# Optimization experiments

Measured on AMD Instinct MI355X. Metric: run time of the kernel, lower is better.

Reference implementation:

```python
import jax, jax.numpy as jnp
import numpy as np

B, S, Lc = 128, 128, 20          # batch, words per sentence, chars per word
AB, E = 100, 64                  # char alphabet, char embedding dim
Hc, H, OUT = 256, 512, 50        # char hidden, word hidden, n tags
PAD = 0                          # padding idx for words and chars


def _cell_params(key, din, h):
    k1, k2, k3, k4 = jax.random.split(key, 4)
    return (jax.random.normal(k1, (4 * h, din)) * 0.05,
            jax.random.normal(k2, (4 * h, h)) * 0.05,
            jax.random.normal(k3, (4 * h,)) * 0.05,
            jax.random.normal(k4, (4 * h,)) * 0.05)


def setup_inputs() -> dict:
    key = jax.random.key(0)
    ks = jax.random.split(key, 12)
    x = jax.random.randint(ks[0], (B, S, Lc), 0, AB)
    emb = jax.random.normal(ks[1], (AB, E)) * 0.05
    emb = emb.at[PAD].set(0.0)  # nn.Embedding padding_idx row is zero
    cW_ih, cW_hh, cb_ih, cb_hh = _cell_params(ks[2], E, Hc)
    fW_ih, fW_hh, fb_ih, fb_hh = _cell_params(ks[3], Hc, H)
    bW_ih, bW_hh, bb_ih, bb_hh = _cell_params(ks[4], Hc, H)
    W1 = jax.random.normal(ks[5], (256, 2 * H)) * 0.05
    b1 = jax.random.normal(ks[6], (256,)) * 0.05
    W2 = jax.random.normal(ks[7], (256, 256)) * 0.05
    b2 = jax.random.normal(ks[8], (256,)) * 0.05
    W3 = jax.random.normal(ks[9], (OUT, 256)) * 0.05
    b3 = jax.random.normal(ks[10], (OUT,)) * 0.05
    return dict(x=x, emb=emb,
                cW_ih=cW_ih, cW_hh=cW_hh, cb_ih=cb_ih, cb_hh=cb_hh,
                fW_ih=fW_ih, fW_hh=fW_hh, fb_ih=fb_ih, fb_hh=fb_hh,
                bW_ih=bW_ih, bW_hh=bW_hh, bb_ih=bb_ih, bb_hh=bb_hh,
                W1=W1, b1=b1, W2=W2, b2=b2, W3=W3, b3=b3)


def _lstm_cell(x_t, h, c, W_ih, W_hh, b_ih, b_hh):
    # PyTorch LSTMCell: gates ordered i, f, g, o
    g = x_t @ W_ih.T + b_ih + h @ W_hh.T + b_hh
    i, f, gg, o = jnp.split(g, 4, axis=-1)
    c = jax.nn.sigmoid(f) * c + jax.nn.sigmoid(i) * jnp.tanh(gg)
    h = jax.nn.sigmoid(o) * jnp.tanh(c)
    return h, c


def _char_acceptor(e_seq, lengths, W_ih, W_hh, b_ih, b_hh, hsize):
    # e_seq: [N, T, E]; returns last non-padded hidden state per row: [N, hsize]
    N, T, _ = e_seq.shape
    h0 = jnp.zeros((N, hsize), e_seq.dtype)

    def step(carry, inp):
        h, c, last = carry
        x_t, t = inp
        h, c = _lstm_cell(x_t, h, c, W_ih, W_hh, b_ih, b_hh)
        last = jnp.where((lengths > t)[:, None], h, last)
        return (h, c, last), None

    xs = (jnp.swapaxes(e_seq, 0, 1), jnp.arange(T))
    (_, _, last), _ = jax.lax.scan(step, (h0, h0, h0), xs)
    return last


def _lstm_transduce(seq_tbd, W_ih, W_hh, b_ih, b_hh, hsize):
    # seq_tbd: [T, B, D] -> all hidden states [T, B, hsize]
    Tb = seq_tbd.shape[1]
    h0 = jnp.zeros((Tb, hsize), seq_tbd.dtype)

    def step(carry, x_t):
        h, c = carry
        h, c = _lstm_cell(x_t, h, c, W_ih, W_hh, b_ih, b_hh)
        return (h, c), h

    _, hs = jax.lax.scan(step, (h0, h0), seq_tbd)
    return hs


def reference(x, emb,
              cW_ih, cW_hh, cb_ih, cb_hh,
              fW_ih, fW_hh, fb_ih, fb_hh,
              bW_ih, bW_hh, bb_ih, bb_hh,
              W1, b1, W2, b2, W3, b3):
    Bx, Sx, Lx = x.shape
    xf = x.reshape(Bx * Sx, Lx)                       # all words flattened
    e = emb[xf]                                       # [B*S, Lc, E]
    lengths = (xf != PAD).sum(axis=1)
    char_out = _char_acceptor(e, lengths, cW_ih, cW_hh, cb_ih, cb_hh, Hc)
    word_seq = char_out.reshape(Bx, Sx, Hc)           # [B, S, Hc]

    seq_tbd = jnp.swapaxes(word_seq, 0, 1)            # [S, B, Hc]
    hs_f = _lstm_transduce(seq_tbd, fW_ih, fW_hh, fb_ih, fb_hh, H)
    hs_b = _lstm_transduce(seq_tbd[::-1], bW_ih, bW_hh, bb_ih, bb_hh, H)[::-1]
    hs = jnp.concatenate([hs_f, hs_b], axis=-1)       # [S, B, 2H]
    hs = jnp.swapaxes(hs, 0, 1)                       # [B, S, 2H]

    h1 = jax.nn.relu(hs @ W1.T + b1)
    h2 = jax.nn.relu(h1 @ W2.T + b2)
    logits = h2 @ W3.T + b3                           # [B, S, OUT]
    return jax.nn.log_softmax(logits, axis=2)
```

## Files before the change

kernel.cpp:

```cpp
#include <hip/hip_runtime.h>
#include <hip/hip_bf16.h>
#include <math.h>

typedef __hip_bfloat16 bf16;
typedef __attribute__((ext_vector_type(8))) short bf16x8;
typedef __attribute__((ext_vector_type(4))) float f32x4;
typedef long i64t;

#define NW   16384
#define LC   20
#define EDIM 64
#define HC   256
#define HW   512
#define SEQ  128
#define NOUT 50
#define NWB  64
#define FPAD 16

#define LOG2E 1.4426950408889634f
__device__ __forceinline__ float fex2(float x) {
  float r; asm("v_exp_f32 %0, %1" : "=v"(r) : "v"(x)); return r;
}
__device__ __forceinline__ float frcp(float x) {
  float r; asm("v_rcp_f32 %0, %1" : "=v"(r) : "v"(x)); return r;
}
__device__ __forceinline__ float flog2(float x) {
  float r; asm("v_log_f32 %0, %1" : "=v"(r) : "v"(x)); return r;
}
__device__ __forceinline__ float fsig(float x) { return frcp(1.f + fex2(-LOG2E * x)); }
__device__ __forceinline__ float ftanh(float x) {
  return 1.f - 2.f * frcp(1.f + fex2(2.f * LOG2E * x));
}

__device__ __forceinline__ unsigned short f2bu(float f) {
  bf16 h = __float2bfloat16(f);
  return *reinterpret_cast<unsigned short*>(&h);
}
__device__ __forceinline__ bf16x8 ld8(const unsigned short* p) {
  return *reinterpret_cast<const bf16x8*>(p);
}
__device__ __forceinline__ float fp8_to_f32(unsigned int b) {
  float r; asm("v_cvt_f32_fp8 %0, %1" : "=v"(r) : "v"(b)); return r;
}
__device__ __forceinline__ i64t ld8sc8(const unsigned char* p) {
  i64t r;
  asm volatile("global_load_dwordx2 %0, %1, off sc0 sc1" : "=v"(r) : "v"(p));
  return r;
}
__device__ __forceinline__ void st8sc8(unsigned char* p, i64t v) {
  asm volatile("global_store_dwordx2 %0, %1, off sc0 sc1" :: "v"(p), "v"(v) : "memory");
}
#define MFMA(a, b, c)  __builtin_amdgcn_mfma_f32_16x16x32_bf16(a, b, c, 0, 0, 0)
#define MFMA8(a, b, c) __builtin_amdgcn_mfma_f32_16x16x32_fp8_fp8(a, b, c, 0, 0, 0)

__global__ __launch_bounds__(512, 1) void char_lstm(
    const int* __restrict__ x, const unsigned char* __restrict__ emb8,
    const unsigned char* __restrict__ Wc8, const float* __restrict__ bcT,
    unsigned short* __restrict__ lastT, const int* __restrict__ len) {
  __shared__ unsigned char Hs8[2][64][264];
  __shared__ _Float16 Cs[256][66];
  __shared__ int lenS[64];
  const int tid = threadIdx.x;
  const int w = tid >> 6, l = tid & 63;
  const int l16 = l & 15, lk8 = (l >> 4) * 8, q = l >> 4;
  const int w0 = blockIdx.x * 64;
  if (tid < 64) lenS[tid] = len[w0 + tid];

  for (int t = 0; t < LC; ++t) {
    const int cur = t & 1, nxt = cur ^ 1;
    int xi[4];
#pragma unroll
    for (int wh = 0; wh < 4; ++wh) xi[wh] = x[(w0 + wh * 16 + l16) * LC + t];
#pragma unroll
    for (int c = 0; c < 2; ++c) {
      const int chg = w * 2 + c;
      const int cc0 = chg * 64;
      f32x4 acc[4][4] = {};
#pragma unroll
      for (int kk = 0; kk < 2; ++kk) {
        const int k = kk * 32 + lk8;
        const unsigned char* wp = Wc8 + (size_t)(cc0 + l16) * 320 + k;
        i64t bv8[4];
#pragma unroll
        for (int g = 0; g < 4; ++g)
          bv8[g] = *reinterpret_cast<const i64t*>(wp + g * 16 * 320);
#pragma unroll
        for (int wh = 0; wh < 4; ++wh) {
          i64t a8 = *reinterpret_cast<const i64t*>(emb8 + (size_t)xi[wh] * 64 + k);
#pragma unroll
          for (int g = 0; g < 4; ++g) acc[wh][g] = MFMA8(bv8[g], a8, acc[wh][g]);
        }
      }
      if (t > 0) {
#pragma unroll
        for (int kk = 2; kk < 10; ++kk) {
          const int k = kk * 32 + lk8;
          const unsigned char* wp = Wc8 + (size_t)(cc0 + l16) * 320 + k;
          i64t bv8[4];
#pragma unroll
          for (int g = 0; g < 4; ++g)
            bv8[g] = *reinterpret_cast<const i64t*>(wp + g * 16 * 320);
#pragma unroll
          for (int wh = 0; wh < 4; ++wh) {
            i64t a8 = *reinterpret_cast<const i64t*>(&Hs8[cur][wh * 16 + l16][k - 64]);
#pragma unroll
            for (int g = 0; g < 4; ++g) acc[wh][g] = MFMA8(bv8[g], a8, acc[wh][g]);
          }
        }
      }
      float4 bb4[4];
#pragma unroll
      for (int e = 0; e < 4; ++e)
        bb4[e] = *reinterpret_cast<const float4*>(bcT + (chg * 16 + q * 4 + e) * 4);
      const int uoff = chg * 16 + q * 4;
#pragma unroll
      for (int wh = 0; wh < 4; ++wh) {
        const int wd = wh * 16 + l16;
        float hv[4];
#pragma unroll
        for (int e = 0; e < 4; ++e) {
          const int ug = chg * 16 + q * 4 + e;
          const float gi = acc[wh][0][e] + bb4[e].x;
          const float gf = acc[wh][1][e] + bb4[e].y;
          const float gg = acc[wh][2][e] + bb4[e].z;
          const float go = acc[wh][3][e] + bb4[e].w;
          const float cprev = t ? (float)Cs[ug][wd] : 0.f;
          const float ccv = fsig(gf) * cprev + fsig(gi) * ftanh(gg);
          Cs[ug][wd] = (_Float16)ccv;
          hv[e] = fsig(go) * ftanh(ccv);
        }
        const int d0 = __builtin_amdgcn_cvt_pk_fp8_f32(hv[0], hv[1], 0, false);
        const int d1 = __builtin_amdgcn_cvt_pk_fp8_f32(hv[2], hv[3], 0, false);
        const unsigned int pk = (unsigned int)(d0 & 0xFFFF) |
                                ((unsigned int)(d1 & 0xFFFF) << 16);
        *reinterpret_cast<unsigned int*>(&Hs8[nxt][wd][uoff]) = pk;
      }
    }
    __syncthreads();
    {
      const int wd = tid >> 3, sub = tid & 7;
      const int myl = lenS[wd];
      if (myl == t + 1 || (myl == 0 && t == 0)) {
        const int n = w0 + wd;
        const int lrow = ((n & 127) * 128 + (n >> 7)) * HC;
        if (myl == 0) {
          bf16x8 z = {};
#pragma unroll
          for (int j = 0; j < 4; ++j)
            *reinterpret_cast<bf16x8*>(lastT + lrow + sub * 32 + j * 8) = z;
        } else {
#pragma unroll
          for (int j = 0; j < 4; ++j) {
            unsigned int v0 = *reinterpret_cast<unsigned int*>(
                &Hs8[nxt][wd][sub * 32 + j * 8]);
            unsigned int v1 = *reinterpret_cast<unsigned int*>(
                &Hs8[nxt][wd][sub * 32 + j * 8 + 4]);
            union { unsigned short s[8]; bf16x8 v; } o;
#pragma unroll
            for (int b = 0; b < 4; ++b) {
              o.s[b]     = f2bu(fp8_to_f32((v0 >> (8 * b)) & 0xFF));
              o.s[4 + b] = f2bu(fp8_to_f32((v1 >> (8 * b)) & 0xFF));
            }
            *reinterpret_cast<bf16x8*>(lastT + lrow + sub * 32 + j * 8) = o.v;
          }
        }
      }
    }
  }
}

__global__ __launch_bounds__(256, 1) void word_lstm(
    const unsigned short* __restrict__ lastT,
    const unsigned short* __restrict__ W16,
    const unsigned short* __restrict__ W16b,
    const unsigned char* __restrict__ W8f,
    const unsigned char* __restrict__ W8b,
    const float* __restrict__ bfi, const float* __restrict__ bbi,
    unsigned char* __restrict__ hbL8,
    unsigned short* __restrict__ hsW,
    int* __restrict__ aflag) {
  __shared__ unsigned short Wlds16[64 * 256];
  __shared__ unsigned char  Wlds8[64 * 512];
  __shared__ unsigned short ht[128][24];
  __shared__ unsigned char  ht8[128][24];
  const int tid = threadIdx.x;
  const int w = tid >> 6, l = tid & 63;
  const int l16 = l & 15, lk8 = (l >> 4) * 8, q = l >> 4;
  const int dir = blockIdx.x >> 5;
  const int nb = blockIdx.x & 31;
  const int c0 = nb * 64;
  const unsigned short* Wx = dir ? W16b : W16;
  const unsigned char*  Wh = dir ? W8b : W8f;
  const float* bias = dir ? bbi : bfi;
  for (int ci = tid; ci < 64 * 32; ci += 256) {
    const int col = ci >> 5, kc = (ci & 31) * 8;
    const int kcs = kc ^ ((col & 15) * 8);
    *reinterpret_cast<bf16x8*>(&Wlds16[col * 256 + kcs]) =
        ld8(Wx + (size_t)(c0 + col) * 768 + kc);
  }
  for (int ci = tid; ci < 64 * 64; ci += 256) {
    const int col = ci >> 6, kb = (ci & 63) * 8;
    const int kbs = kb ^ ((col & 15) * 8);
    *reinterpret_cast<i64t*>(&Wlds8[col * 512 + kbs]) =
        *reinterpret_cast<const i64t*>(Wh + (size_t)(c0 + col) * 512 + kb);
  }
  const float b0 = bias[c0 + 0 * 16 + l16];
  const float b1 = bias[c0 + 1 * 16 + l16];
  const float b2 = bias[c0 + 2 * 16 + l16];
  const float b3 = bias[c0 + 3 * 16 + l16];
  const int ksw = l16 * 8;
  float cst[8];
#pragma unroll
  for (int i = 0; i < 8; ++i) cst[i] = 0.f;
  __syncthreads();

  for (int t = 0; t < SEQ; ++t) {
    const int cur = t & 1;
    const int pos = dir ? (SEQ - 1 - t) : t;
    f32x4 acc[2][4] = {};
#pragma unroll
    for (int kk = 0; kk < 8; ++kk) {
      const int k = kk * 32 + lk8;
      bf16x8 a0 = ld8(lastT + ((size_t)pos * 128 + w * 32 + l16) * HC + k);
      bf16x8 a1 = ld8(lastT + ((size_t)pos * 128 + w * 32 + l16 + 16) * HC + k);
      const int ks = k ^ ksw;
#pragma unroll
      for (int nn = 0; nn < 4; ++nn) {
        bf16x8 bv = ld8(&Wlds16[(l16 + nn * 16) * 256 + ks]);
        acc[0][nn] = MFMA(a0, bv, acc[0][nn]);
        acc[1][nn] = MFMA(a1, bv, acc[1][nn]);
      }
    }
    if (t > 0) {
      if (w == 0) {
        const int* fp = aflag + (size_t)(dir * SEQ + (t - 1)) * 32 * FPAD;
        for (;;) {
          int v = 1;
          if (l < 32)
            v = __hip_atomic_load(fp + l * FPAD, __ATOMIC_RELAXED,
                                  __HIP_MEMORY_SCOPE_AGENT);
          if (__ballot(v != 0) == ~0ull) break;
          __builtin_amdgcn_s_sleep(1);
        }
      }
      __syncthreads();
      i64t af8[16][2];
      const unsigned char* hp =
          hbL8 + (size_t)(((cur ^ 1) * 2 + dir) * 32) * 128 * 16;
#pragma unroll
      for (int kk = 0; kk < 16; ++kk) {
        const int u = kk * 32 + lk8;
        const int nbs = u >> 4, ul = u & 15;
#pragma unroll
        for (int r = 0; r < 2; ++r) {
          const int bt = w * 32 + l16 + r * 16;
          af8[kk][r] = ld8sc8(hp + ((size_t)nbs * 128 + bt) * 16 + ul);
        }
      }
      asm volatile("s_waitcnt vmcnt(0)" ::: "memory");
      __builtin_amdgcn_sched_barrier(0);
#pragma unroll
      for (int kk = 0; kk < 16; ++kk) {
        const int ks8 = (kk * 32 + lk8) ^ ksw;
#pragma unroll
        for (int nn = 0; nn < 4; ++nn) {
          i64t w8 = *reinterpret_cast<const i64t*>(
              &Wlds8[(l16 + nn * 16) * 512 + ks8]);
          acc[0][nn] = MFMA8(af8[kk][0], w8, acc[0][nn]);
          acc[1][nn] = MFMA8(af8[kk][1], w8, acc[1][nn]);
        }
      }
    }
    float hvf[8];
    int bats[8];
#pragma unroll
    for (int m = 0; m < 2; ++m)
#pragma unroll
      for (int e = 0; e < 4; ++e) {
        const int j = m * 4 + e;
        const float gi = acc[m][0][e] + b0;
        const float gf = acc[m][1][e] + b1;
        const float gg = acc[m][2][e] + b2;
        const float go = acc[m][3][e] + b3;
        const float ccv = fsig(gf) * cst[j] + fsig(gi) * ftanh(gg);
        cst[j] = ccv;
        const float hv = fsig(go) * ftanh(ccv);
        const int bat = w * 32 + q * 4 + e + m * 16;
        ht[bat][l16] = f2bu(hv);
        hvf[j] = hv; bats[j] = bat;
      }
    {
      const int d0 = __builtin_amdgcn_cvt_pk_fp8_f32(hvf[0], hvf[1], 0, false);
      const int d1 = __builtin_amdgcn_cvt_pk_fp8_f32(hvf[2], hvf[3], 0, false);
      const int d2 = __builtin_amdgcn_cvt_pk_fp8_f32(hvf[4], hvf[5], 0, false);
      const int d3 = __builtin_amdgcn_cvt_pk_fp8_f32(hvf[6], hvf[7], 0, false);
      ht8[bats[0]][l16] = (unsigned char)(d0 & 255);
      ht8[bats[1]][l16] = (unsigned char)((d0 >> 8) & 255);
      ht8[bats[2]][l16] = (unsigned char)(d1 & 255);
      ht8[bats[3]][l16] = (unsigned char)((d1 >> 8) & 255);
      ht8[bats[4]][l16] = (unsigned char)(d2 & 255);
      ht8[bats[5]][l16] = (unsigned char)((d2 >> 8) & 255);
      ht8[bats[6]][l16] = (unsigned char)(d3 & 255);
      ht8[bats[7]][l16] = (unsigned char)((d3 >> 8) & 255);
    }
    __syncthreads();
    const int ub = tid >> 1, uh = tid & 1;
    i64t hv8 = *reinterpret_cast<const i64t*>(&ht8[ub][uh * 8]);
    st8sc8(hbL8 + (size_t)((cur * 2 + dir) * 32 + nb) * 128 * 16
               + ub * 16 + uh * 8, hv8);
    if (t < SEQ - 1) {
      asm volatile("s_waitcnt vmcnt(0)" ::: "memory");
      __syncthreads();
      if (tid == 0)
        __hip_atomic_store(aflag + ((size_t)(dir * SEQ + t) * 32 + nb) * FPAD, 1,
                           __ATOMIC_RELAXED, __HIP_MEMORY_SCOPE_AGENT);
    }
    bf16x8 hv = ld8(&ht[ub][uh * 8]);
    *reinterpret_cast<bf16x8*>(
        hsW + (((size_t)(dir * 32 + nb) * 128 + pos) * 128 + ub) * 16 + uh * 8) = hv;
  }
}

__global__ __launch_bounds__(256) void mlp1_gemm(
    const unsigned short* __restrict__ hsW, const unsigned short* __restrict__ W1b,
    const float* __restrict__ bias, unsigned short* __restrict__ out) {
  const int tid = threadIdx.x;
  const int w = tid >> 6, l = tid & 63;
  const int l16 = l & 15, lk8 = (l >> 4) * 8;
  const int by = blockIdx.y;
  const int row0 = by * 128 + w * 32;
  const int col0 = blockIdx.x * 64;
  f32x4 acc[2][4] = {};
  for (int kk = 0; kk < 32; ++kk) {
    const int k = kk * 32 + lk8;
    const int dirk = k >> 9, u = k & 511, nbs = u >> 4, ul = u & 15;
    const int p0 = w * 32 + l16, p1 = p0 + 16;
    bf16x8 a0 = ld8(hsW + (((size_t)(dirk * 32 + nbs) * 128 + p0) * 128 + by) * 16 + ul);
    bf16x8 a1 = ld8(hsW + (((size_t)(dirk * 32 + nbs) * 128 + p1) * 128 + by) * 16 + ul);
    const unsigned short* wp = W1b + (size_t)(col0 + l16) * 1024 + k;
#pragma unroll
    for (int nn = 0; nn < 4; ++nn) {
      bf16x8 bv = ld8(wp + nn * 16 * 1024);
      acc[0][nn] = MFMA(a0, bv, acc[0][nn]);
      acc[1][nn] = MFMA(a1, bv, acc[1][nn]);
    }
  }
  const int cr = (l >> 4) * 4;
#pragma unroll
  for (int m = 0; m < 2; ++m)
#pragma unroll
    for (int nn = 0; nn < 4; ++nn)
#pragma unroll
      for (int e = 0; e < 4; ++e) {
        const int r = row0 + m * 16 + cr + e;
        const int c = col0 + nn * 16 + l16;
        out[(size_t)r * 256 + c] = f2bu(fmaxf(acc[m][nn][e] + bias[c], 0.f));
      }
}

__global__ __launch_bounds__(256) void mlp_gemm(
    const unsigned short* __restrict__ A, int lda,
    const unsigned short* __restrict__ W, int ldw,
    const float* __restrict__ bias, unsigned short* __restrict__ out,
    int ldo, int nk, int relu) {
  const int tid = threadIdx.x;
  const int w = tid >> 6, l = tid & 63;
  const int l16 = l & 15, lk8 = (l >> 4) * 8;
  const int row0 = blockIdx.y * 128 + w * 32;
  const int col0 = blockIdx.x * 64;
  f32x4 acc[2][4] = {};
  for (int kk = 0; kk < nk; ++kk) {
    const int k = kk * 32 + lk8;
    bf16x8 a0 = ld8(A + (size_t)(row0 + l16) * lda + k);
    bf16x8 a1 = ld8(A + (size_t)(row0 + 16 + l16) * lda + k);
    const unsigned short* wp = W + (size_t)(col0 + l16) * ldw + k;
    bf16x8 bb[4];
#pragma unroll
    for (int nn = 0; nn < 4; ++nn) bb[nn] = ld8(wp + nn * 16 * ldw);
#pragma unroll
    for (int nn = 0; nn < 4; ++nn) {
      acc[0][nn] = MFMA(a0, bb[nn], acc[0][nn]);
      acc[1][nn] = MFMA(a1, bb[nn], acc[1][nn]);
    }
  }
  const int cr = (l >> 4) * 4;
#pragma unroll
  for (int m = 0; m < 2; ++m)
#pragma unroll
    for (int nn = 0; nn < 4; ++nn)
#pragma unroll
      for (int e = 0; e < 4; ++e) {
        const int r = row0 + m * 16 + cr + e;
        const int c = col0 + nn * 16 + l16;
        float v = acc[m][nn][e] + bias[c];
        if (relu) v = fmaxf(v, 0.f);
        out[(size_t)r * ldo + c] = f2bu(v);
      }
}

__global__ __launch_bounds__(256) void logits_fused(
    const unsigned short* __restrict__ h2, const unsigned short* __restrict__ W3p,
    const float* __restrict__ b3, float* __restrict__ out) {
  __shared__ float gt[128][68];
  __shared__ float lseb[128];
  const int tid = threadIdx.x;
  const int w = tid >> 6, l = tid & 63;
  const int l16 = l & 15, lk8 = (l >> 4) * 8;
  const int r0 = blockIdx.x * 128;
  const int rr0 = w * 32 + l16, rr1 = rr0 + 16;
  f32x4 acc[2][4] = {};
#pragma unroll
  for (int kk = 0; kk < 8; ++kk) {
    const int k = kk * 32 + lk8;
    bf16x8 a0 = ld8(h2 + (size_t)(r0 + rr0) * 256 + k);
    bf16x8 a1 = ld8(h2 + (size_t)(r0 + rr1) * 256 + k);
#pragma unroll
    for (int nn = 0; nn < 4; ++nn) {
      bf16x8 bv = ld8(W3p + (size_t)(nn * 16 + l16) * 256 + k);
      acc[0][nn] = MFMA(a0, bv, acc[0][nn]);
      acc[1][nn] = MFMA(a1, bv, acc[1][nn]);
    }
  }
  const int cr = (l >> 4) * 4;
#pragma unroll
  for (int m = 0; m < 2; ++m)
#pragma unroll
    for (int nn = 0; nn < 4; ++nn)
#pragma unroll
      for (int e = 0; e < 4; ++e) {
        const int col = nn * 16 + l16;
        gt[w * 32 + m * 16 + cr + e][col] =
            acc[m][nn][e] + (col < NOUT ? b3[col] : 0.f);
      }
  __syncthreads();
  if (tid < 128) {
    float mx = -INFINITY;
#pragma unroll
    for (int j = 0; j < NOUT; ++j) mx = fmaxf(mx, gt[tid][j]);
    float s = 0.f;
#pragma unroll
    for (int j = 0; j < NOUT; ++j) s += fex2(LOG2E * (gt[tid][j] - mx));
    lseb[tid] = flog2(s) * 0.6931471805599453f + mx;
  }
  __syncthreads();
  for (int idx = tid; idx < 128 * NOUT; idx += 256) {
    const int r = idx / NOUT, j = idx - r * NOUT;
    out[(size_t)(r0 + r) * NOUT + j] = gt[r][j] - lseb[r];
  }
}

__global__ void prep_w(const float* __restrict__ ih, const float* __restrict__ hh,
                       unsigned short* __restrict__ dst, int HU, int KI, int KH) {
  const int K = KI + KH;
  const long tot = (long)HU * 4 * K;
  for (long idx = (long)blockIdx.x * blockDim.x + threadIdx.x; idx < tot;
       idx += (long)gridDim.x * blockDim.x) {
    const int row = (int)(idx / K), k = (int)(idx % K);
    const int chunk = row >> 6, c = row & 63;
    const int g = c >> 4, u = chunk * 16 + (c & 15);
    const float v = (k < KI) ? ih[(size_t)(g * HU + u) * KI + k]
                             : hh[(size_t)(g * HU + u) * KH + (k - KI)];
    dst[idx] = f2bu(v);
  }
}

__global__ void prep_wc8(const float* __restrict__ ih, const float* __restrict__ hh,
                         unsigned char* __restrict__ dst, int HU, int KI, int KH) {
  const int K = KI + KH;
  const long tot = (long)HU * 4 * (K / 2);
  for (long p = (long)blockIdx.x * blockDim.x + threadIdx.x; p < tot;
       p += (long)gridDim.x * blockDim.x) {
    const int row = (int)(p / (K / 2)), kp = (int)(p % (K / 2)) * 2;
    const int chunk = row >> 6, c = row & 63;
    const int g = c >> 4, u = chunk * 16 + (c & 15);
    const float a = (kp < KI) ? ih[(size_t)(g * HU + u) * KI + kp]
                              : hh[(size_t)(g * HU + u) * KH + (kp - KI)];
    const float b = (kp + 1 < KI) ? ih[(size_t)(g * HU + u) * KI + kp + 1]
                                  : hh[(size_t)(g * HU + u) * KH + (kp + 1 - KI)];
    const int d = __builtin_amdgcn_cvt_pk_fp8_f32(a, b, 0, false);
    *reinterpret_cast<unsigned short*>(dst + (size_t)row * K + kp) =
        (unsigned short)(d & 0xFFFF);
  }
}

__global__ void prep_w8(const float* __restrict__ hh, unsigned char* __restrict__ dst,
                        int HU, int KH) {
  const long tot = (long)HU * 4 * (KH / 2);
  for (long p = (long)blockIdx.x * blockDim.x + threadIdx.x; p < tot;
       p += (long)gridDim.x * blockDim.x) {
    const int row = (int)(p / (KH / 2)), kp = (int)(p % (KH / 2)) * 2;
    const int chunk = row >> 6, c = row & 63;
    const int g = c >> 4, u = chunk * 16 + (c & 15);
    const float a = hh[(size_t)(g * HU + u) * KH + kp];
    const float b = hh[(size_t)(g * HU + u) * KH + kp + 1];
    const int d = __builtin_amdgcn_cvt_pk_fp8_f32(a, b, 0, false);
    *reinterpret_cast<unsigned short*>(dst + (size_t)row * KH + kp) =
        (unsigned short)(d & 0xFFFF);
  }
}

__global__ void prep_bias(const float* bih, const float* bhh, float* dst, int HU) {
  const int idx = blockIdx.x * blockDim.x + threadIdx.x;
  if (idx < 4 * HU) {
    const int chunk = idx >> 6, c = idx & 63;
    const int g = c >> 4, u = chunk * 16 + (c & 15);
    dst[idx] = bih[g * HU + u] + bhh[g * HU + u];
  }
}

__global__ void prep_biasT(const float* bih, const float* bhh, float* dst, int HU) {
  const int idx = blockIdx.x * blockDim.x + threadIdx.x;
  if (idx < 4 * HU) {
    const int u = idx >> 2, g = idx & 3;
    dst[idx] = bih[g * HU + u] + bhh[g * HU + u];
  }
}

__global__ void conv_bf(const float* __restrict__ src, unsigned short* __restrict__ dst,
                        long n) {
  for (long i = (long)blockIdx.x * blockDim.x + threadIdx.x; i < n;
       i += (long)gridDim.x * blockDim.x)
    dst[i] = f2bu(src[i]);
}

__global__ void conv_fp8(const float* __restrict__ src, unsigned char* __restrict__ dst,
                         long n2) {
  for (long i = (long)blockIdx.x * blockDim.x + threadIdx.x; i < n2;
       i += (long)gridDim.x * blockDim.x) {
    const int d = __builtin_amdgcn_cvt_pk_fp8_f32(src[i * 2], src[i * 2 + 1], 0, false);
    *reinterpret_cast<unsigned short*>(dst + i * 2) = (unsigned short)(d & 0xFFFF);
  }
}

__global__ void prep_w3(const float* __restrict__ W3, unsigned short* __restrict__ dst) {
  const int i = blockIdx.x * blockDim.x + threadIdx.x;
  if (i < 64 * 256) {
    const int r = i >> 8;
    dst[i] = (r < NOUT) ? f2bu(W3[i]) : 0;
  }
}

__global__ void lengths_k(const int* x, int* len) {
  const int n = blockIdx.x * blockDim.x + threadIdx.x;
  if (n < NW) {
    int c = 0;
#pragma unroll
    for (int l = 0; l < LC; ++l) c += (x[(size_t)n * LC + l] != 0) ? 1 : 0;
    len[n] = c;
  }
}

__global__ void zero_k(int* p, int n) {
  const int i = blockIdx.x * blockDim.x + threadIdx.x;
  if (i < n) p[i] = 0;
}

__global__ void sentinel_k(float* out, int n) {
  const int i = blockIdx.x * blockDim.x + threadIdx.x;
  if (i < n) out[i] = 1000.0f;
}

extern "C" void kernel_launch(void* const* d_in, const int* in_sizes, int n_in,
                              void* d_out, int out_size, void* d_ws, size_t ws_size,
                              hipStream_t stream) {
  const int*   x     = (const int*)d_in[0];
  const float* emb   = (const float*)d_in[1];
  const float* cW_ih = (const float*)d_in[2];
  const float* cW_hh = (const float*)d_in[3];
  const float* cb_ih = (const float*)d_in[4];
  const float* cb_hh = (const float*)d_in[5];
  const float* fW_ih = (const float*)d_in[6];
  const float* fW_hh = (const float*)d_in[7];
  const float* fb_ih = (const float*)d_in[8];
  const float* fb_hh = (const float*)d_in[9];
  const float* bW_ih = (const float*)d_in[10];
  const float* bW_hh = (const float*)d_in[11];
  const float* bb_ih = (const float*)d_in[12];
  const float* bb_hh = (const float*)d_in[13];
  const float* W1 = (const float*)d_in[14];
  const float* b1 = (const float*)d_in[15];
  const float* W2 = (const float*)d_in[16];
  const float* b2 = (const float*)d_in[17];
  const float* W3 = (const float*)d_in[18];
  const float* b3 = (const float*)d_in[19];
  float* out = (float*)d_out;
  (void)in_sizes; (void)n_in;

  char* ws = (char*)d_ws;
  size_t off = 0;
  auto alloc = [&](size_t bytes) -> char* {
    char* p = ws + off;
    off += (bytes + 255) & ~(size_t)255;
    return p;
  };
  int*            len_  = (int*)alloc((size_t)NW * 4);
  int*            aflag = (int*)alloc((size_t)2 * SEQ * 32 * FPAD * 4);
  unsigned char*  emb8  = (unsigned char*)alloc((size_t)100 * EDIM);
  unsigned char*  Wc8   = (unsigned char*)alloc((size_t)1024 * 320);
  unsigned short* Wf_i  = (unsigned short*)alloc((size_t)2048 * 768 * 2);
  unsigned short* Wb_i  = (unsigned short*)alloc((size_t)2048 * 768 * 2);
  unsigned char*  Wf8   = (unsigned char*)alloc((size_t)2048 * 512);
  unsigned char*  Wb8   = (unsigned char*)alloc((size_t)2048 * 512);
  unsigned short* W1b   = (unsigned short*)alloc((size_t)256 * 1024 * 2);
  unsigned short* W2b   = (unsigned short*)alloc((size_t)256 * 256 * 2);
  unsigned short* W3p   = (unsigned short*)alloc((size_t)64 * 256 * 2);
  float*          bcT   = (float*)alloc(1024 * 4);
  float*          bf_i  = (float*)alloc(2048 * 4);
  float*          bb_i  = (float*)alloc(2048 * 4);
  unsigned short* lastT = (unsigned short*)alloc((size_t)NW * HC * 2);
  unsigned char*  hbL8  = (unsigned char*)alloc((size_t)2 * 2 * 32 * 128 * 16);
  unsigned short* hsW   = (unsigned short*)alloc((size_t)2 * 32 * 128 * 128 * 16 * 2);
  unsigned short* h1    = (unsigned short*)alloc((size_t)NW * HC * 2);
  unsigned short* h2    = (unsigned short*)alloc((size_t)NW * HC * 2);

  if (off > ws_size) {
    sentinel_k<<<(out_size + 255) / 256, 256, 0, stream>>>(out, out_size);
    return;
  }

  auto cdiv = [](long a, long b) { return (int)((a + b - 1) / b); };

  prep_wc8<<<640, 256, 0, stream>>>(cW_ih, cW_hh, Wc8, HC, EDIM, HC);
  prep_w<<<3072, 256, 0, stream>>>(fW_ih, fW_hh, Wf_i, HW, HC, HW);
  prep_w<<<3072, 256, 0, stream>>>(bW_ih, bW_hh, Wb_i, HW, HC, HW);
  prep_w8<<<2048, 256, 0, stream>>>(fW_hh, Wf8, HW, HW);
  prep_w8<<<2048, 256, 0, stream>>>(bW_hh, Wb8, HW, HW);
  prep_biasT<<<cdiv(1024, 256), 256, 0, stream>>>(cb_ih, cb_hh, bcT, HC);
  prep_bias<<<cdiv(2048, 256), 256, 0, stream>>>(fb_ih, fb_hh, bf_i, HW);
  prep_bias<<<cdiv(2048, 256), 256, 0, stream>>>(bb_ih, bb_hh, bb_i, HW);
  conv_fp8<<<13, 256, 0, stream>>>(emb, emb8, 100L * EDIM / 2);
  conv_bf<<<1024, 256, 0, stream>>>(W1, W1b, 256L * 1024);
  conv_bf<<<256, 256, 0, stream>>>(W2, W2b, 256L * 256);
  prep_w3<<<64, 256, 0, stream>>>(W3, W3p);
  lengths_k<<<cdiv(NW, 256), 256, 0, stream>>>(x, len_);
  zero_k<<<cdiv(2 * SEQ * 32 * FPAD, 256), 256, 0, stream>>>(aflag, 2 * SEQ * 32 * FPAD);

  char_lstm<<<NW / 64, 512, 0, stream>>>(x, emb8, Wc8, bcT, lastT, len_);

  word_lstm<<<NWB, 256, 0, stream>>>(lastT, Wf_i, Wb_i, Wf8, Wb8, bf_i, bb_i,
                                     hbL8, hsW, aflag);

  mlp1_gemm<<<dim3(4, 128), 256, 0, stream>>>(hsW, W1b, b1, h1);
  mlp_gemm<<<dim3(4, 128), 256, 0, stream>>>(h1, 256, W2b, 256, b2, h2, 256, 8, 1);
  logits_fused<<<NW / 128, 256, 0, stream>>>(h2, W3p, b3, out);
}
```

Before: 1.372 ms.

## Place word-LSTM directions on single XCDs and use cheaper cache scope when co-located

The word LSTM now launches 256 blocks and keeps only those with blockIdx%8 in {0,1}. With round-robin block dispatch this is meant to put all 32 blocks of one direction on the same XCD. Each block reads its XCD id from a hardware register, counts co-residents, and when all 32 share an XCD it uses sc0-only (L2-coherent) loads and stores for the recurrent state and flags instead of sc0 sc1 system-scope accesses. This aims to cut per-step cross-block synchronisation latency. The input-weight prep also drops the unused recurrent half of the bf16 matrix, shrinking that buffer and prep kernel. The speed path depends on the undocumented block-to-XCD mapping, with fallback to the old coherent path otherwise.

```diff
diff --git a/kernel.cpp b/kernel.cpp
--- a/kernel.cpp
+++ b/kernel.cpp
@@ -14,7 +14,6 @@
 #define HW   512
 #define SEQ  128
 #define NOUT 50
-#define NWB  64
 #define FPAD 16
 
 #define LOG2E 1.4426950408889634f
@@ -42,13 +41,25 @@
 __device__ __forceinline__ float fp8_to_f32(unsigned int b) {
   float r; asm("v_cvt_f32_fp8 %0, %1" : "=v"(r) : "v"(b)); return r;
 }
-__device__ __forceinline__ i64t ld8sc8(const unsigned char* p) {
+__device__ __forceinline__ i64t ld8x(const unsigned char* p, bool f) {
   i64t r;
-  asm volatile("global_load_dwordx2 %0, %1, off sc0 sc1" : "=v"(r) : "v"(p));
+  if (f) asm volatile("global_load_dwordx2 %0, %1, off sc0" : "=v"(r) : "v"(p));
+  else   asm volatile("global_load_dwordx2 %0, %1, off sc0 sc1" : "=v"(r) : "v"(p));
   return r;
 }
-__device__ __forceinline__ void st8sc8(unsigned char* p, i64t v) {
-  asm volatile("global_store_dwordx2 %0, %1, off sc0 sc1" :: "v"(p), "v"(v) : "memory");
+__device__ __forceinline__ void st8x(unsigned char* p, i64t v, bool f) {
+  if (f) asm volatile("global_store_dwordx2 %0, %1, off sc0" :: "v"(p), "v"(v) : "memory");
+  else   asm volatile("global_store_dwordx2 %0, %1, off sc0 sc1" :: "v"(p), "v"(v) : "memory");
+}
+__device__ __forceinline__ int ldflagx(const int* p, bool f) {
+  int r;
+  if (f) asm volatile("global_load_dword %0, %1, off sc0" : "=v"(r) : "v"(p));
+  else   asm volatile("global_load_dword %0, %1, off sc0 sc1" : "=v"(r) : "v"(p));
+  return r;
+}
+__device__ __forceinline__ void stflagx(int* p, int v, bool f) {
+  if (f) asm volatile("global_store_dword %0, %1, off sc0" :: "v"(p), "v"(v) : "memory");
+  else   asm volatile("global_store_dword %0, %1, off sc0 sc1" :: "v"(p), "v"(v) : "memory");
 }
 #define MFMA(a, b, c)  __builtin_amdgcn_mfma_f32_16x16x32_bf16(a, b, c, 0, 0, 0)
 #define MFMA8(a, b, c) __builtin_amdgcn_mfma_f32_16x16x32_fp8_fp8(a, b, c, 0, 0, 0)
@@ -179,24 +190,37 @@
     unsigned char* __restrict__ hbL8,
     unsigned short* __restrict__ hsW,
     int* __restrict__ aflag) {
+  const int bx = blockIdx.x;
+  if ((bx & 7) > 1) return;
   __shared__ unsigned short Wlds16[64 * 256];
   __shared__ unsigned char  Wlds8[64 * 512];
   __shared__ unsigned short ht[128][24];
   __shared__ unsigned char  ht8[128][24];
+  __shared__ int fastS;
   const int tid = threadIdx.x;
   const int w = tid >> 6, l = tid & 63;
   const int l16 = l & 15, lk8 = (l >> 4) * 8, q = l >> 4;
-  const int dir = blockIdx.x >> 5;
-  const int nb = blockIdx.x & 31;
+  const int dir = bx & 7;
+  const int nb = bx >> 3;
   const int c0 = nb * 64;
   const unsigned short* Wx = dir ? W16b : W16;
   const unsigned char*  Wh = dir ? W8b : W8f;
   const float* bias = dir ? bbi : bfi;
+  int* negcnt = aflag + (size_t)2 * SEQ * 32 * FPAD;
+  if (tid == 0) {
+    const int xcc = __builtin_amdgcn_s_getreg(20 | (31 << 11)) & 7;
+    int* xc = negcnt + 16 + dir * 8 + xcc;
+    __hip_atomic_fetch_add(xc, 1, __ATOMIC_RELAXED, __HIP_MEMORY_SCOPE_AGENT);
+    __hip_atomic_fetch_add(negcnt, 1, __ATOMIC_RELAXED, __HIP_MEMORY_SCOPE_AGENT);
+    while (__hip_atomic_load(negcnt, __ATOMIC_RELAXED, __HIP_MEMORY_SCOPE_AGENT) < 64)
+      __builtin_amdgcn_s_sleep(2);
+    fastS = (__hip_atomic_load(xc, __ATOMIC_RELAXED, __HIP_MEMORY_SCOPE_AGENT) == 32);
+  }
   for (int ci = tid; ci < 64 * 32; ci += 256) {
     const int col = ci >> 5, kc = (ci & 31) * 8;
     const int kcs = kc ^ ((col & 15) * 8);
     *reinterpret_cast<bf16x8*>(&Wlds16[col * 256 + kcs]) =
-        ld8(Wx + (size_t)(c0 + col) * 768 + kc);
+        ld8(Wx + (size_t)(c0 + col) * 256 + kc);
   }
   for (int ci = tid; ci < 64 * 64; ci += 256) {
     const int col = ci >> 6, kb = (ci & 63) * 8;
@@ -213,6 +237,7 @@
 #pragma unroll
   for (int i = 0; i < 8; ++i) cst[i] = 0.f;
   __syncthreads();
+  const bool fast = (fastS != 0);
 
   for (int t = 0; t < SEQ; ++t) {
     const int cur = t & 1;
@@ -236,9 +261,7 @@
         const int* fp = aflag + (size_t)(dir * SEQ + (t - 1)) * 32 * FPAD;
         for (;;) {
           int v = 1;
-          if (l < 32)
-            v = __hip_atomic_load(fp + l * FPAD, __ATOMIC_RELAXED,
-                                  __HIP_MEMORY_SCOPE_AGENT);
+          if (l < 32) v = ldflagx(fp + l * FPAD, fast);
           if (__ballot(v != 0) == ~0ull) break;
           __builtin_amdgcn_s_sleep(1);
         }
@@ -254,7 +277,7 @@
 #pragma unroll
         for (int r = 0; r < 2; ++r) {
           const int bt = w * 32 + l16 + r * 16;
-          af8[kk][r] = ld8sc8(hp + ((size_t)nbs * 128 + bt) * 16 + ul);
+          af8[kk][r] = ld8x(hp + ((size_t)nbs * 128 + bt) * 16 + ul, fast);
         }
       }
       asm volatile("s_waitcnt vmcnt(0)" ::: "memory");
@@ -306,14 +329,13 @@
     __syncthreads();
     const int ub = tid >> 1, uh = tid & 1;
     i64t hv8 = *reinterpret_cast<const i64t*>(&ht8[ub][uh * 8]);
-    st8sc8(hbL8 + (size_t)((cur * 2 + dir) * 32 + nb) * 128 * 16
-               + ub * 16 + uh * 8, hv8);
+    st8x(hbL8 + (size_t)((cur * 2 + dir) * 32 + nb) * 128 * 16
+             + ub * 16 + uh * 8, hv8, fast);
     if (t < SEQ - 1) {
       asm volatile("s_waitcnt vmcnt(0)" ::: "memory");
       __syncthreads();
       if (tid == 0)
-        __hip_atomic_store(aflag + ((size_t)(dir * SEQ + t) * 32 + nb) * FPAD, 1,
-                           __ATOMIC_RELAXED, __HIP_MEMORY_SCOPE_AGENT);
+        stflagx(aflag + ((size_t)(dir * SEQ + t) * 32 + nb) * FPAD, 1, fast);
     }
     bf16x8 hv = ld8(&ht[ub][uh * 8]);
     *reinterpret_cast<bf16x8*>(
@@ -449,18 +471,15 @@
   }
 }
 
-__global__ void prep_w(const float* __restrict__ ih, const float* __restrict__ hh,
-                       unsigned short* __restrict__ dst, int HU, int KI, int KH) {
-  const int K = KI + KH;
-  const long tot = (long)HU * 4 * K;
+__global__ void prep_wx(const float* __restrict__ ih, unsigned short* __restrict__ dst,
+                        int HU, int KI) {
+  const long tot = (long)HU * 4 * KI;
   for (long idx = (long)blockIdx.x * blockDim.x + threadIdx.x; idx < tot;
        idx += (long)gridDim.x * blockDim.x) {
-    const int row = (int)(idx / K), k = (int)(idx % K);
+    const int row = (int)(idx / KI), k = (int)(idx % KI);
     const int chunk = row >> 6, c = row & 63;
     const int g = c >> 4, u = chunk * 16 + (c & 15);
-    const float v = (k < KI) ? ih[(size_t)(g * HU + u) * KI + k]
-                             : hh[(size_t)(g * HU + u) * KH + (k - KI)];
-    dst[idx] = f2bu(v);
+    dst[idx] = f2bu(ih[(size_t)(g * HU + u) * KI + k]);
   }
 }
 
@@ -593,12 +612,13 @@
     off += (bytes + 255) & ~(size_t)255;
     return p;
   };
+  const int NFLAG = 2 * SEQ * 32 * FPAD + 32;
   int*            len_  = (int*)alloc((size_t)NW * 4);
-  int*            aflag = (int*)alloc((size_t)2 * SEQ * 32 * FPAD * 4);
+  int*            aflag = (int*)alloc((size_t)NFLAG * 4);
   unsigned char*  emb8  = (unsigned char*)alloc((size_t)100 * EDIM);
   unsigned char*  Wc8   = (unsigned char*)alloc((size_t)1024 * 320);
-  unsigned short* Wf_i  = (unsigned short*)alloc((size_t)2048 * 768 * 2);
-  unsigned short* Wb_i  = (unsigned short*)alloc((size_t)2048 * 768 * 2);
+  unsigned short* Wf_i  = (unsigned short*)alloc((size_t)2048 * 256 * 2);
+  unsigned short* Wb_i  = (unsigned short*)alloc((size_t)2048 * 256 * 2);
   unsigned char*  Wf8   = (unsigned char*)alloc((size_t)2048 * 512);
   unsigned char*  Wb8   = (unsigned char*)alloc((size_t)2048 * 512);
   unsigned short* W1b   = (unsigned short*)alloc((size_t)256 * 1024 * 2);
@@ -621,8 +641,8 @@
   auto cdiv = [](long a, long b) { return (int)((a + b - 1) / b); };
 
   prep_wc8<<<640, 256, 0, stream>>>(cW_ih, cW_hh, Wc8, HC, EDIM, HC);
-  prep_w<<<3072, 256, 0, stream>>>(fW_ih, fW_hh, Wf_i, HW, HC, HW);
-  prep_w<<<3072, 256, 0, stream>>>(bW_ih, bW_hh, Wb_i, HW, HC, HW);
+  prep_wx<<<1024, 256, 0, stream>>>(fW_ih, Wf_i, HW, HC);
+  prep_wx<<<1024, 256, 0, stream>>>(bW_ih, Wb_i, HW, HC);
   prep_w8<<<2048, 256, 0, stream>>>(fW_hh, Wf8, HW, HW);
   prep_w8<<<2048, 256, 0, stream>>>(bW_hh, Wb8, HW, HW);
   prep_biasT<<<cdiv(1024, 256), 256, 0, stream>>>(cb_ih, cb_hh, bcT, HC);
@@ -633,11 +653,11 @@
   conv_bf<<<256, 256, 0, stream>>>(W2, W2b, 256L * 256);
   prep_w3<<<64, 256, 0, stream>>>(W3, W3p);
   lengths_k<<<cdiv(NW, 256), 256, 0, stream>>>(x, len_);
-  zero_k<<<cdiv(2 * SEQ * 32 * FPAD, 256), 256, 0, stream>>>(aflag, 2 * SEQ * 32 * FPAD);
+  zero_k<<<cdiv(NFLAG, 256), 256, 0, stream>>>(aflag, NFLAG);
 
   char_lstm<<<NW / 64, 512, 0, stream>>>(x, emb8, Wc8, bcT, lastT, len_);
 
-  word_lstm<<<NWB, 256, 0, stream>>>(lastT, Wf_i, Wb_i, Wf8, Wb8, bf_i, bb_i,
+  word_lstm<<<256, 256, 0, stream>>>(lastT, Wf_i, Wb_i, Wf8, Wb8, bf_i, bb_i,
                                      hbL8, hsW, aflag);
 
   mlp1_gemm<<<dim3(4, 128), 256, 0, stream>>>(hsW, W1b, b1, h1);
```

After: 1.292 ms. 5.9% less time.
